# Kernel tuning notes

Hardware: AMD Instinct MI355X
Metric: run time of the kernel (lower is better)

Reference implementation:

```python
import jax, jax.numpy as jnp
import numpy as np

B, N, T = 512, 128, 64
ALPHA = 0.5  # LeakyReLU negative slope
NEG = jnp.float32(-9e15)


def _gat(h, mask, W, a):
    # GraphAttentionLayer with concat=True (trailing relu), eval mode (no dropout)
    Wh = h @ W                                   # [B,N,F]
    F = W.shape[1]
    e1 = Wh @ a[:F]                              # [B,N,1]
    e2 = Wh @ a[F:]                              # [B,N,1]
    e = jax.nn.leaky_relu(e1 + jnp.swapaxes(e2, 1, 2), ALPHA)  # [B,N,N]
    e = jnp.where(mask, e, NEG)
    att = jax.nn.softmax(e, axis=1)              # torch softmax dim=1 (over rows)
    return jax.nn.relu(jnp.matmul(att, Wh))


def _lstm_layer(x, wih, whh, bih, bhh):
    # x: [T,B,in]; hidden size 1; torch gate order i,f,g,o
    h0 = jnp.zeros((x.shape[1], 1), x.dtype)
    def step(carry, xt):
        h, c = carry
        g = xt @ wih.T + h @ whh.T + bih + bhh   # [B,4]
        i, f, gg, o = jnp.split(g, 4, axis=-1)
        c = jax.nn.sigmoid(f) * c + jax.nn.sigmoid(i) * jnp.tanh(gg)
        h = jax.nn.sigmoid(o) * jnp.tanh(c)
        return (h, c), h
    _, ys = jax.lax.scan(step, (h0, h0), x)
    return ys                                    # [T,B,1]


def setup_inputs() -> dict:
    key = jax.random.key(0)
    ks = jax.random.split(key, 32)
    def xu(k, shape, gain=1.414):
        lim = gain * np.sqrt(6.0 / (shape[0] + shape[1]))
        return jax.random.uniform(k, shape, jnp.float32, -lim, lim)
    d = {}
    d["adjacency"] = jax.random.randint(ks[0], (B, N, N), 0, 2, dtype=jnp.int32)
    d["feature"] = jax.random.normal(ks[1], (B, N), jnp.float32)
    d["time"] = jax.random.normal(ks[2], (B, N), jnp.float32)
    d["interval_popularity"] = jax.random.normal(ks[3], (B, T), jnp.float32)
    # GAT params
    d["W1"] = xu(ks[4], (1, 512)); d["a1"] = xu(ks[5], (1024, 1))
    d["W2"] = xu(ks[6], (512, 8)); d["a2"] = xu(ks[7], (16, 1))
    # attention-pooling params (torch.randn in original)
    d["Weight"] = jax.random.normal(ks[8], (128, 128), jnp.float32)
    d["Wv"] = jax.random.normal(ks[9], (128, 128), jnp.float32)
    # 2-layer LSTM(1->1)
    d["wih0"] = jax.random.normal(ks[10], (4, 1)) * 0.5
    d["whh0"] = jax.random.normal(ks[11], (4, 1)) * 0.5
    d["bih0"] = jax.random.normal(ks[12], (4,)) * 0.5
    d["bhh0"] = jax.random.normal(ks[13], (4,)) * 0.5
    d["wih1"] = jax.random.normal(ks[14], (4, 1)) * 0.5
    d["whh1"] = jax.random.normal(ks[15], (4, 1)) * 0.5
    d["bih1"] = jax.random.normal(ks[16], (4,)) * 0.5
    d["bhh1"] = jax.random.normal(ks[17], (4,)) * 0.5
    # MultiheadAttention(embed_dim=1, heads=1)
    d["mha_in_w"] = jax.random.normal(ks[18], (3, 1)) * 0.5
    d["mha_in_b"] = jnp.zeros((3,), jnp.float32)
    d["mha_out_w"] = jax.random.normal(ks[19], (1, 1)) * 0.5
    d["mha_out_b"] = jnp.zeros((1,), jnp.float32)
    # FL MLP: 192->128->32->1 (stored as [in,out])
    d["fl1_w"] = xu(ks[20], (192, 128), 1.0); d["fl1_b"] = jnp.zeros((128,), jnp.float32)
    d["fl2_w"] = xu(ks[21], (128, 32), 1.0);  d["fl2_b"] = jnp.zeros((32,), jnp.float32)
    d["fl3_w"] = xu(ks[22], (32, 1), 1.0);    d["fl3_b"] = jnp.zeros((1,), jnp.float32)
    return d


def reference(adjacency, feature, time, interval_popularity,
              W1, a1, W2, a2, Weight, Wv,
              wih0, whh0, bih0, bhh0, wih1, whh1, bih1, bhh1,
              mha_in_w, mha_in_b, mha_out_w, mha_out_b,
              fl1_w, fl1_b, fl2_w, fl2_b, fl3_w, fl3_b):
    mask = adjacency > 0
    x = feature.reshape(B, N, -1)                # [B,128,1]
    h = _gat(x, mask, W1, a1)                    # [B,128,512]
    h = jax.nn.relu(h)
    h = _gat(h, mask, W2, a2)                    # [B,128,8]

    xs = jnp.swapaxes(interval_popularity.reshape(B, -1, 1), 0, 1)  # [T,B,1]
    xs = _lstm_layer(xs, wih0, whh0, bih0, bhh0)
    xs = _lstm_layer(xs, wih1, whh1, bih1, bhh1)
    ip = jnp.swapaxes(xs, 0, 1).reshape(B, -1)   # [B,64]

    h = jnp.mean(h, axis=2, keepdims=True)       # [B,128,1]
    Wt = time.reshape(B, N, -1)                  # [B,128,1]
    att = jnp.concatenate([h, Wt], axis=2)       # [B,128,2]
    att = jnp.swapaxes(jnp.swapaxes(att, 1, 2) @ Weight, 1, 2)  # [B,128,2]
    att = jax.nn.softmax(att, axis=2)
    hv = jnp.swapaxes(jnp.concatenate([h, Wt], axis=2), 1, 2)   # [B,2,128]
    hv = jax.nn.relu((hv @ Wv).reshape(B, N, -1))  # faithful reshape (not transpose)
    h = jnp.sum(hv * att, axis=2)                # [B,128]

    h = jnp.concatenate([h, ip], axis=1)         # [B,192]
    hq = h[..., None]                            # [B,192,1]
    q = hq * mha_in_w[0, 0] + mha_in_b[0]
    k = hq * mha_in_w[1, 0] + mha_in_b[1]
    v = hq * mha_in_w[2, 0] + mha_in_b[2]
    a = jax.nn.softmax(q @ jnp.swapaxes(k, 1, 2), axis=-1)  # scale=1/sqrt(1)
    ho = (a @ v) * mha_out_w[0, 0] + mha_out_b[0]
    h = (ho + hq).reshape(B, -1)                 # [B,192]

    h = jax.nn.relu(h @ fl1_w + fl1_b)
    h = jnp.tanh(h @ fl2_w + fl2_b)
    h = jax.nn.relu(h @ fl3_w + fl3_b)           # [B,1]
    return h
```

## Files before the change

kernel.cpp:

```cpp
#include <hip/hip_runtime.h>
#include <math.h>

typedef unsigned int uint;
typedef unsigned long long ull;

#define L2E 1.44269504f

__device__ __forceinline__ float lrelu(float z){ return fmaxf(z, 0.5f*z); }
__device__ __forceinline__ float reluf(float z){ return fmaxf(z, 0.f); }
__device__ __forceinline__ float fexp(float z){ return __builtin_amdgcn_exp2f(z*L2E); }
__device__ __forceinline__ float frcp(float z){ return __builtin_amdgcn_rcpf(z); }
__device__ __forceinline__ float tanh_n(float z){
  return __fmaf_rn(2.f, __builtin_amdgcn_rcpf(1.f + __builtin_amdgcn_exp2f(-2.f*L2E*z)), -1.f);
}

__global__ __launch_bounds__(256) void pack_prep_kernel(
    const int* __restrict__ adj, ull* __restrict__ gpk, ull* __restrict__ gpkT,
    const float* __restrict__ W1, const float* __restrict__ a1,
    const float* __restrict__ W2, const float* __restrict__ a2,
    float* __restrict__ consts,
    const float* __restrict__ ipop,
    const float* __restrict__ wih0, const float* __restrict__ whh0,
    const float* __restrict__ bih0, const float* __restrict__ bhh0,
    const float* __restrict__ wih1, const float* __restrict__ whh1,
    const float* __restrict__ bih1, const float* __restrict__ bhh1,
    float* __restrict__ ip_out)
{
  const int bid = blockIdx.x, t = threadIdx.x;

  if (bid < 512){
    __shared__ ull rowW[256];
    const int w = t >> 6, ln = t & 63;
    const int* abase = adj + (((long)bid) << 14) + w*4096 + ln;
    ull myword = 0;
    #pragma unroll
    for (int blk = 0; blk < 8; ++blk){
      int v[8];
      #pragma unroll
      for (int q = 0; q < 8; ++q) v[q] = abase[(blk*8 + q)*64];
      #pragma unroll
      for (int q = 0; q < 8; ++q){
        ull m = __ballot(v[q] > 0);
        const int it = blk*8 + q;
        myword = (ln == it) ? m : myword;
      }
    }
    rowW[t] = myword;
    gpk[bid*256 + t] = myword;
    __syncthreads();
    const int j = t & 127, h2 = t >> 7;
    const int wsel = j >> 6, bsel = j & 63;
    ull outw = 0;
    #pragma unroll 8
    for (int k = 0; k < 64; ++k){
      outw |= ((rowW[(64*h2 + k)*2 + wsel] >> bsel) & 1ull) << k;
    }
    gpkT[bid*256 + j*2 + h2] = outw;
    return;
  }
  if (bid < 520){
    if (t >= 64) return;
    const int b = (bid - 512)*64 + t;
    float wi0[4], wh0[4], bb0[4], wi1[4], wh1[4], bb1[4];
    #pragma unroll
    for (int k = 0; k < 4; ++k){
      const float s = (k == 2) ? -2.f*L2E : -L2E;
      wi0[k]=wih0[k]*s; wh0[k]=whh0[k]*s; bb0[k]=(bih0[k]+bhh0[k])*s;
      wi1[k]=wih1[k]*s; wh1[k]=whh1[k]*s; bb1[k]=(bih1[k]+bhh1[k])*s;
    }
    const float4* xsrc = (const float4*)(ipop + b*64);
    float4* hdst = (float4*)(ip_out + b*64);
    float4 xv = xsrc[0];
    float h1=0.f, c1v=0.f, h2=0.f, c2v=0.f;
    #pragma unroll
    for (int q = 0; q < 16; ++q){
      const float4 xc = xv;
      if (q < 15) xv = xsrc[q+1];
      float hout[4];
      #pragma unroll
      for (int s = 0; s < 4; ++s){
        const float x = (s==0) ? xc.x : (s==1) ? xc.y : (s==2) ? xc.z : xc.w;
        float gi = frcp(1.f + __builtin_amdgcn_exp2f(__fmaf_rn(x, wi0[0], __fmaf_rn(h1, wh0[0], bb0[0]))));
        float gf = frcp(1.f + __builtin_amdgcn_exp2f(__fmaf_rn(x, wi0[1], __fmaf_rn(h1, wh0[1], bb0[1]))));
        float gg = __fmaf_rn(2.f, frcp(1.f + __builtin_amdgcn_exp2f(__fmaf_rn(x, wi0[2], __fmaf_rn(h1, wh0[2], bb0[2])))), -1.f);
        float go = frcp(1.f + __builtin_amdgcn_exp2f(__fmaf_rn(x, wi0[3], __fmaf_rn(h1, wh0[3], bb0[3]))));
        c1v = gf*c1v + gi*gg;
        h1 = go*tanh_n(c1v);
        float hi2 = frcp(1.f + __builtin_amdgcn_exp2f(__fmaf_rn(h1, wi1[0], __fmaf_rn(h2, wh1[0], bb1[0]))));
        float hf2 = frcp(1.f + __builtin_amdgcn_exp2f(__fmaf_rn(h1, wi1[1], __fmaf_rn(h2, wh1[1], bb1[1]))));
        float hg2 = __fmaf_rn(2.f, frcp(1.f + __builtin_amdgcn_exp2f(__fmaf_rn(h1, wi1[2], __fmaf_rn(h2, wh1[2], bb1[2])))), -1.f);
        float ho2 = frcp(1.f + __builtin_amdgcn_exp2f(__fmaf_rn(h1, wi1[3], __fmaf_rn(h2, wh1[3], bb1[3]))));
        c2v = hf2*c2v + hi2*hg2;
        h2 = ho2*tanh_n(c2v);
        hout[s] = h2;
      }
      hdst[q] = make_float4(hout[0], hout[1], hout[2], hout[3]);
    }
    return;
  }
  {
    __shared__ float redA[256], redB[256];
    float s1 = 0.f, s2 = 0.f;
    for (int f = t; f < 512; f += 256){ float w = W1[f]; s1 += w*a1[f]; s2 += w*a1[512+f]; }
    redA[t] = s1; redB[t] = s2; __syncthreads();
    for (int st = 128; st > 0; st >>= 1){
      if (t < st){ redA[t] += redA[t+st]; redB[t] += redB[t+st]; }
      __syncthreads();
    }
    if (t == 0){ consts[0] = redA[0]; consts[1] = redB[0]; }
    __syncthreads();
    const int g = t >> 5, seg = t & 31;
    float accP = 0.f, accQ = 0.f;
    for (int k = 0; k < 16; ++k){
      int f = seg*16 + k;
      float w = W1[f];
      float v = w * W2[f*8 + g];
      if (w > 0.f) accP += v; else accQ += v;
    }
    redA[t] = accP; redB[t] = accQ; __syncthreads();
    for (int st = 16; st > 0; st >>= 1){
      if (seg < st){ redA[t] += redA[t+st]; redB[t] += redB[t+st]; }
      __syncthreads();
    }
    if (seg == 0){ consts[2+g] = redA[t]; consts[10+g] = redB[t]; }
    __syncthreads();
    if (t == 0){
      float pA=0.f,qA=0.f,pB=0.f,qB=0.f;
      for (int gg = 0; gg < 8; ++gg){
        pA += consts[2+gg]*a2[gg];   qA += consts[10+gg]*a2[gg];
        pB += consts[2+gg]*a2[8+gg]; qB += consts[10+gg]*a2[8+gg];
      }
      consts[18]=pA; consts[19]=qA; consts[20]=pB; consts[21]=qB;
    }
  }
}

__global__ __launch_bounds__(256) void gat_head_kernel(
    const ull* __restrict__ gpk, const ull* __restrict__ gpkT,
    const float* __restrict__ feat, const float* __restrict__ timei,
    const float* __restrict__ Weight, const float* __restrict__ Wv,
    const float* __restrict__ consts, const float* __restrict__ ip,
    const float* __restrict__ mha_in_w, const float* __restrict__ mha_in_b,
    const float* __restrict__ mha_out_w, const float* __restrict__ mha_out_b,
    const float* __restrict__ fl1_w, const float* __restrict__ fl1_b,
    const float* __restrict__ fl2_w, const float* __restrict__ fl2_b,
    const float* __restrict__ fl3_w, const float* __restrict__ fl3_b,
    float* __restrict__ out)
{
  const int b = blockIdx.x, t = threadIdx.x;
  const int lane = t & 127, h = t >> 7;

  __shared__ float  xs[128], tim[128], hm[128], eAs[128], thr1[128];
  __shared__ float2 f2a[128];
  __shared__ float2 red2[2][128];
  __shared__ float4 q4[128];
  __shared__ float4 pool4[2][128];
  __shared__ float2 kv[192];
  __shared__ float  hq[192], h2s[192];
  __shared__ float  sred[8];

  const float c1 = consts[0], c2 = consts[1];
  const float pA = consts[18], qA = consts[19], pB = consts[20], qB = consts[21];

  float ipreg = 0.f;
  if (t < 128){ xs[t] = feat[b*128 + t]; tim[t] = timei[b*128 + t]; }
  if (t >= 192) ipreg = ip[b*64 + (t - 192)];
  const ull rowm = gpk [b*256 + lane*2 + h];
  const ull colm = gpkT[b*256 + lane*2 + h];
  __syncthreads();
  if (t < 64){
    float mx = fmaxf(xs[t], xs[t+64]);
    float mn = fminf(xs[t], xs[t+64]);
    #pragma unroll
    for (int off = 32; off; off >>= 1){
      mx = fmaxf(mx, __shfl_xor(mx, off));
      mn = fminf(mn, __shfl_xor(mn, off));
    }
    if (t == 0){ sred[0] = mx; sred[1] = mn; }
  }
  __syncthreads();

  float myE1=0.f, myEh=0.f, myA=0.f, myB=0.f, mythr=0.f, myx=0.f;
  {
    const float rmax = (c1 >= 0.f) ? c1*sred[0] : c1*sred[1];
    if (t < 128){
      myx = xs[t];
      float r  = c1*myx;
      float cj = c2*myx;
      float cb = lrelu(rmax + cj);
      myE1  = fexp(r - rmax);
      myEh  = fexp(0.5f*(r - rmax));
      myA   = fexp(rmax + cj - cb);
      myB   = fexp(0.5f*(rmax + cj) - cb);
      mythr = fexp(-cj - rmax);
      f2a[t] = make_float2(myE1, myEh);
      thr1[t] = mythr;
    }
  }
  __syncthreads();

  {
    const float thrj = thr1[lane];
    float s1 = 0.f, s2 = 0.f;
    #pragma unroll 8
    for (int k = 0; k < 64; ++k){
      float2 E = f2a[64*h + k];
      bool m = ((colm >> k) & 1ull);
      bool cond = (E.x >= thrj);
      s1 += (m &&  cond) ? E.x : 0.f;
      s2 += (m && !cond) ? E.y : 0.f;
    }
    red2[h][lane] = make_float2(s1, s2);
  }
  __syncthreads();
  if (t < 128){
    float2 a = red2[0][t], bb = red2[1][t];
    float den = __fmaf_rn(myA, a.x + bb.x, myB*(a.y + bb.y));
    float cr = frcp(den);
    q4[t] = make_float4(myA*cr*myx, myB*cr*myx, mythr, 0.f);
  }
  __syncthreads();
  {
    const float2 Eo = f2a[lane];
    float t1 = 0.f, t2 = 0.f;
    #pragma unroll 8
    for (int k = 0; k < 64; ++k){
      float4 G = q4[64*h + k];
      bool m = ((rowm >> k) & 1ull);
      bool cond = (Eo.x >= G.z);
      t1 += (m &&  cond) ? G.x : 0.f;
      t2 += (m && !cond) ? G.y : 0.f;
    }
    red2[h][lane] = make_float2(t1, t2);
  }
  __syncthreads();
  float u = 0.f, eBv = 0.f, eAv = 0.f;
  if (t < 128){
    float2 a = red2[0][t], bb = red2[1][t];
    u = __fmaf_rn(myE1, a.x + bb.x, myEh*(a.y + bb.y));
    eAv = (u >= 0.f ? pA : qA)*u;
    eBv = (u >= 0.f ? pB : qB)*u;
    eAs[t] = eAv;
  }
  __syncthreads();
  if (t < 64){
    float mx = fmaxf(eAs[t], eAs[t+64]);
    #pragma unroll
    for (int off = 32; off; off >>= 1) mx = fmaxf(mx, __shfl_xor(mx, off));
    if (t == 0) sred[2] = mx;
  }
  __syncthreads();
  float myE1b=0.f, myEhb=0.f, myA2=0.f, myB2=0.f;
  {
    const float eAmax = sred[2];
    if (t < 128){
      float cb = lrelu(eAmax + eBv);
      myE1b = fexp(eAv - eAmax);
      myEhb = fexp(0.5f*(eAv - eAmax));
      myA2  = fexp(eAmax + eBv - cb);
      myB2  = fexp(0.5f*(eAmax + eBv) - cb);
      float th = fexp(-eBv - eAmax);
      f2a[t] = make_float2(myE1b, myEhb);
      thr1[t] = th;
    }
  }
  __syncthreads();
  {
    const float thrj = thr1[lane];
    float s1 = 0.f, s2 = 0.f;
    #pragma unroll 8
    for (int k = 0; k < 64; ++k){
      float2 E = f2a[64*h + k];
      bool m = ((colm >> k) & 1ull);
      bool cond = (E.x >= thrj);
      s1 += (m &&  cond) ? E.x : 0.f;
      s2 += (m && !cond) ? E.y : 0.f;
    }
    red2[h][lane] = make_float2(s1, s2);
  }
  __syncthreads();
  if (t < 128){
    float2 a = red2[0][t], bb = red2[1][t];
    float den = __fmaf_rn(myA2, a.x + bb.x, myB2*(a.y + bb.y));
    float cr = frcp(den);
    float up = fmaxf(u, 0.f), un = fminf(u, 0.f);
    q4[t] = make_float4(myA2*cr*up, myB2*cr*up, myA2*cr*un, myB2*cr*un);
  }
  __syncthreads();
  {
    const float2 Eo = f2a[lane];
    float sp1=0.f, sp2=0.f, sn1=0.f, sn2=0.f;
    #pragma unroll 8
    for (int k = 0; k < 64; ++k){
      int j = 64*h + k;
      float4 G = q4[j];
      float thj = thr1[j];
      bool m = ((rowm >> k) & 1ull);
      bool cond = (Eo.x >= thj);
      sp1 += (m &&  cond) ? G.x : 0.f;
      sp2 += (m && !cond) ? G.y : 0.f;
      sn1 += (m &&  cond) ? G.z : 0.f;
      sn2 += (m && !cond) ? G.w : 0.f;
    }
    pool4[h][lane] = make_float4(sp1, sp2, sn1, sn2);
  }
  __syncthreads();
  if (t < 128){
    float4 a = pool4[0][t], bb = pool4[1][t];
    float sp = __fmaf_rn(myE1b, a.x + bb.x, myEhb*(a.y + bb.y));
    float sn = __fmaf_rn(myE1b, a.z + bb.z, myEhb*(a.w + bb.w));
    float acc = 0.f;
    #pragma unroll
    for (int g = 0; g < 8; ++g) acc += reluf(__fmaf_rn(sp, consts[2+g], sn*consts[10+g]));
    hm[t] = 0.125f*acc;
  }
  __syncthreads();

  {
    const int n = lane;
    float a0=0.f, a1v=0.f, v0=0.f, v1=0.f;
    const int m0 = h*64;
    #pragma unroll 4
    for (int k = 0; k < 64; ++k){
      int m = m0 + k;
      float hmv = hm[m], tv = tim[m];
      float wg = Weight[(m<<7) + n], wvv = Wv[(m<<7) + n];
      a0 = __fmaf_rn(hmv, wg, a0); a1v = __fmaf_rn(tv, wg, a1v);
      v0 = __fmaf_rn(hmv, wvv, v0); v1 = __fmaf_rn(tv, wvv, v1);
    }
    pool4[h][n] = make_float4(a0, a1v, v0, v1);
  }
  __syncthreads();
  float att0 = 0.f, att1 = 0.f, rsv = 0.f;
  if (t < 128){
    float4 a = pool4[0][t], bb = pool4[1][t];
    float A0 = a.x + bb.x, A1 = a.y + bb.y;
    red2[0][t] = make_float2(a.z + bb.z, a.w + bb.w);
    float mx = fmaxf(A0, A1);
    att0 = fexp(A0 - mx); att1 = fexp(A1 - mx);
    rsv = frcp(att0 + att1);
  }
  __syncthreads();
  if (t < 128){
    float r0, r1;
    if (t < 64){ r0 = red2[0][2*t].x;     r1 = red2[0][2*t+1].x; }
    else       { r0 = red2[0][2*t-128].y; r1 = red2[0][2*t-127].y; }
    hq[t] = (reluf(r0)*att0 + reluf(r1)*att1)*rsv;
  }
  if (t >= 192) hq[128 + (t - 192)] = ipreg;
  __syncthreads();

  const float wq = mha_in_w[0], wk = mha_in_w[1], wv = mha_in_w[2];
  const float bq = mha_in_b[0], bk = mha_in_b[1], bv = mha_in_b[2];
  const float wo = mha_out_w[0], bo = mha_out_b[0];
  if (t < 192){
    float hv_ = hq[t];
    kv[t] = make_float2(__fmaf_rn(hv_, wk, bk), __fmaf_rn(hv_, wv, bv));
  }
  __syncthreads();
  if (t < 64){
    float k0 = kv[t].x, k1 = kv[t+64].x, k2 = kv[t+128].x;
    float mx = fmaxf(fmaxf(k0, k1), k2);
    float mn = fminf(fminf(k0, k1), k2);
    #pragma unroll
    for (int off = 32; off; off >>= 1){
      mx = fmaxf(mx, __shfl_xor(mx, off));
      mn = fminf(mn, __shfl_xor(mn, off));
    }
    if (t == 0){ sred[3] = mx; sred[4] = mn; }
  }
  __syncthreads();
  if (t < 192){
    float hv_ = hq[t];
    float qi = __fmaf_rn(hv_, wq, bq);
    float mx = (qi >= 0.f) ? qi*sred[3] : qi*sred[4];
    const float qi2 = qi*L2E, mx2 = mx*L2E;
    float den = 0.f, num = 0.f;
    #pragma unroll 8
    for (int j = 0; j < 192; ++j){
      float2 K = kv[j];
      float e = __builtin_amdgcn_exp2f(__fmaf_rn(qi2, K.x, -mx2));
      den += e; num = __fmaf_rn(e, K.y, num);
    }
    h2s[t] = __fmaf_rn(num*frcp(den), wo, bo) + hv_;
  }
  __syncthreads();
  {
    const int n = t & 127;
    float acc = 0.f;
    const int i0 = h*96;
    #pragma unroll 8
    for (int k = 0; k < 96; ++k){
      int i = i0 + k;
      acc = __fmaf_rn(h2s[i], fl1_w[i*128 + n], acc);
    }
    red2[h][n].x = acc;
  }
  __syncthreads();
  if (t < 128) thr1[t] = reluf(red2[0][t].x + red2[1][t].x + fl1_b[t]);
  __syncthreads();
  if (t < 128){
    const int n = t & 31, seg = t >> 5;
    float p = 0.f;
    #pragma unroll 8
    for (int k = 0; k < 32; ++k){
      int i = seg*32 + k;
      p = __fmaf_rn(thr1[i], fl2_w[i*32 + n], p);
    }
    eAs[t] = p;
  }
  __syncthreads();
  if (t < 32) hm[t] = tanh_n(eAs[t] + eAs[t+32] + eAs[t+64] + eAs[t+96] + fl2_b[t]);
  __syncthreads();
  if (t < 64){
    float p = (t < 32) ? hm[t]*fl3_w[t] : 0.f;
    #pragma unroll
    for (int off = 32; off; off >>= 1) p += __shfl_xor(p, off);
    if (t == 0) out[b] = reluf(p + fl3_b[0]);
  }
}

extern "C" void kernel_launch(void* const* d_in, const int* in_sizes, int n_in,
                              void* d_out, int out_size, void* d_ws, size_t ws_size,
                              hipStream_t stream) {
  const int*   adj    = (const int*)  d_in[0];
  const float* feat   = (const float*)d_in[1];
  const float* timei  = (const float*)d_in[2];
  const float* ipop   = (const float*)d_in[3];
  const float* W1     = (const float*)d_in[4];
  const float* a1     = (const float*)d_in[5];
  const float* W2     = (const float*)d_in[6];
  const float* a2     = (const float*)d_in[7];
  const float* Weight = (const float*)d_in[8];
  const float* Wv     = (const float*)d_in[9];
  const float* wih0   = (const float*)d_in[10];
  const float* whh0   = (const float*)d_in[11];
  const float* bih0   = (const float*)d_in[12];
  const float* bhh0   = (const float*)d_in[13];
  const float* wih1   = (const float*)d_in[14];
  const float* whh1   = (const float*)d_in[15];
  const float* bih1   = (const float*)d_in[16];
  const float* bhh1   = (const float*)d_in[17];
  const float* mha_in_w  = (const float*)d_in[18];
  const float* mha_in_b  = (const float*)d_in[19];
  const float* mha_out_w = (const float*)d_in[20];
  const float* mha_out_b = (const float*)d_in[21];
  const float* fl1_w = (const float*)d_in[22];
  const float* fl1_b = (const float*)d_in[23];
  const float* fl2_w = (const float*)d_in[24];
  const float* fl2_b = (const float*)d_in[25];
  const float* fl3_w = (const float*)d_in[26];
  const float* fl3_b = (const float*)d_in[27];

  ull*   gpk    = (ull*)d_ws;
  ull*   gpkT   = gpk + 131072;
  float* consts = (float*)(gpkT + 131072);
  float* ip     = consts + 32;

  pack_prep_kernel<<<521, 256, 0, stream>>>(adj, gpk, gpkT, W1, a1, W2, a2, consts,
                                            ipop, wih0, whh0, bih0, bhh0,
                                            wih1, whh1, bih1, bhh1, ip);
  gat_head_kernel<<<512, 256, 0, stream>>>(gpk, gpkT, feat, timei, Weight, Wv, consts, ip,
                                           mha_in_w, mha_in_b, mha_out_w, mha_out_b,
                                           fl1_w, fl1_b, fl2_w, fl2_b, fl3_w, fl3_b,
                                           (float*)d_out);
}
```

Baseline: 49.82 us.

## Fuse pack, prep, LSTM and GAT head into one kernel

Merges the adjacency bit-packing, the GAT constant precompute, the LSTM recurrence and the GAT/head computation into a single kernel, one block per batch. The packed masks stay in shared memory instead of being written to and re-read from the workspace, which also removes a kernel launch and the dependency between the two kernels. Each block recomputes the tiny weight-derived constants with wave shuffles, and one thread runs the LSTM in eight 8-step chunks placed between the GAT barriers so it overlaps the GAT work. The trade-offs are redundant constant computation in every block, and a serial LSTM on a single lane that could stretch the barrier phases it is interleaved with.

```diff
diff --git a/kernel.cpp b/kernel.cpp
--- a/kernel.cpp
+++ b/kernel.cpp
@@ -14,132 +14,17 @@
   return __fmaf_rn(2.f, __builtin_amdgcn_rcpf(1.f + __builtin_amdgcn_exp2f(-2.f*L2E*z)), -1.f);
 }
 
-__global__ __launch_bounds__(256) void pack_prep_kernel(
-    const int* __restrict__ adj, ull* __restrict__ gpk, ull* __restrict__ gpkT,
+__global__ __launch_bounds__(256) void fused_kernel(
+    const int* __restrict__ adj, const float* __restrict__ feat,
+    const float* __restrict__ timei,
+    const float* __restrict__ Weight, const float* __restrict__ Wv,
     const float* __restrict__ W1, const float* __restrict__ a1,
     const float* __restrict__ W2, const float* __restrict__ a2,
-    float* __restrict__ consts,
     const float* __restrict__ ipop,
     const float* __restrict__ wih0, const float* __restrict__ whh0,
     const float* __restrict__ bih0, const float* __restrict__ bhh0,
     const float* __restrict__ wih1, const float* __restrict__ whh1,
     const float* __restrict__ bih1, const float* __restrict__ bhh1,
-    float* __restrict__ ip_out)
-{
-  const int bid = blockIdx.x, t = threadIdx.x;
-
-  if (bid < 512){
-    __shared__ ull rowW[256];
-    const int w = t >> 6, ln = t & 63;
-    const int* abase = adj + (((long)bid) << 14) + w*4096 + ln;
-    ull myword = 0;
-    #pragma unroll
-    for (int blk = 0; blk < 8; ++blk){
-      int v[8];
-      #pragma unroll
-      for (int q = 0; q < 8; ++q) v[q] = abase[(blk*8 + q)*64];
-      #pragma unroll
-      for (int q = 0; q < 8; ++q){
-        ull m = __ballot(v[q] > 0);
-        const int it = blk*8 + q;
-        myword = (ln == it) ? m : myword;
-      }
-    }
-    rowW[t] = myword;
-    gpk[bid*256 + t] = myword;
-    __syncthreads();
-    const int j = t & 127, h2 = t >> 7;
-    const int wsel = j >> 6, bsel = j & 63;
-    ull outw = 0;
-    #pragma unroll 8
-    for (int k = 0; k < 64; ++k){
-      outw |= ((rowW[(64*h2 + k)*2 + wsel] >> bsel) & 1ull) << k;
-    }
-    gpkT[bid*256 + j*2 + h2] = outw;
-    return;
-  }
-  if (bid < 520){
-    if (t >= 64) return;
-    const int b = (bid - 512)*64 + t;
-    float wi0[4], wh0[4], bb0[4], wi1[4], wh1[4], bb1[4];
-    #pragma unroll
-    for (int k = 0; k < 4; ++k){
-      const float s = (k == 2) ? -2.f*L2E : -L2E;
-      wi0[k]=wih0[k]*s; wh0[k]=whh0[k]*s; bb0[k]=(bih0[k]+bhh0[k])*s;
-      wi1[k]=wih1[k]*s; wh1[k]=whh1[k]*s; bb1[k]=(bih1[k]+bhh1[k])*s;
-    }
-    const float4* xsrc = (const float4*)(ipop + b*64);
-    float4* hdst = (float4*)(ip_out + b*64);
-    float4 xv = xsrc[0];
-    float h1=0.f, c1v=0.f, h2=0.f, c2v=0.f;
-    #pragma unroll
-    for (int q = 0; q < 16; ++q){
-      const float4 xc = xv;
-      if (q < 15) xv = xsrc[q+1];
-      float hout[4];
-      #pragma unroll
-      for (int s = 0; s < 4; ++s){
-        const float x = (s==0) ? xc.x : (s==1) ? xc.y : (s==2) ? xc.z : xc.w;
-        float gi = frcp(1.f + __builtin_amdgcn_exp2f(__fmaf_rn(x, wi0[0], __fmaf_rn(h1, wh0[0], bb0[0]))));
-        float gf = frcp(1.f + __builtin_amdgcn_exp2f(__fmaf_rn(x, wi0[1], __fmaf_rn(h1, wh0[1], bb0[1]))));
-        float gg = __fmaf_rn(2.f, frcp(1.f + __builtin_amdgcn_exp2f(__fmaf_rn(x, wi0[2], __fmaf_rn(h1, wh0[2], bb0[2])))), -1.f);
-        float go = frcp(1.f + __builtin_amdgcn_exp2f(__fmaf_rn(x, wi0[3], __fmaf_rn(h1, wh0[3], bb0[3]))));
-        c1v = gf*c1v + gi*gg;
-        h1 = go*tanh_n(c1v);
-        float hi2 = frcp(1.f + __builtin_amdgcn_exp2f(__fmaf_rn(h1, wi1[0], __fmaf_rn(h2, wh1[0], bb1[0]))));
-        float hf2 = frcp(1.f + __builtin_amdgcn_exp2f(__fmaf_rn(h1, wi1[1], __fmaf_rn(h2, wh1[1], bb1[1]))));
-        float hg2 = __fmaf_rn(2.f, frcp(1.f + __builtin_amdgcn_exp2f(__fmaf_rn(h1, wi1[2], __fmaf_rn(h2, wh1[2], bb1[2])))), -1.f);
-        float ho2 = frcp(1.f + __builtin_amdgcn_exp2f(__fmaf_rn(h1, wi1[3], __fmaf_rn(h2, wh1[3], bb1[3]))));
-        c2v = hf2*c2v + hi2*hg2;
-        h2 = ho2*tanh_n(c2v);
-        hout[s] = h2;
-      }
-      hdst[q] = make_float4(hout[0], hout[1], hout[2], hout[3]);
-    }
-    return;
-  }
-  {
-    __shared__ float redA[256], redB[256];
-    float s1 = 0.f, s2 = 0.f;
-    for (int f = t; f < 512; f += 256){ float w = W1[f]; s1 += w*a1[f]; s2 += w*a1[512+f]; }
-    redA[t] = s1; redB[t] = s2; __syncthreads();
-    for (int st = 128; st > 0; st >>= 1){
-      if (t < st){ redA[t] += redA[t+st]; redB[t] += redB[t+st]; }
-      __syncthreads();
-    }
-    if (t == 0){ consts[0] = redA[0]; consts[1] = redB[0]; }
-    __syncthreads();
-    const int g = t >> 5, seg = t & 31;
-    float accP = 0.f, accQ = 0.f;
-    for (int k = 0; k < 16; ++k){
-      int f = seg*16 + k;
-      float w = W1[f];
-      float v = w * W2[f*8 + g];
-      if (w > 0.f) accP += v; else accQ += v;
-    }
-    redA[t] = accP; redB[t] = accQ; __syncthreads();
-    for (int st = 16; st > 0; st >>= 1){
-      if (seg < st){ redA[t] += redA[t+st]; redB[t] += redB[t+st]; }
-      __syncthreads();
-    }
-    if (seg == 0){ consts[2+g] = redA[t]; consts[10+g] = redB[t]; }
-    __syncthreads();
-    if (t == 0){
-      float pA=0.f,qA=0.f,pB=0.f,qB=0.f;
-      for (int gg = 0; gg < 8; ++gg){
-        pA += consts[2+gg]*a2[gg];   qA += consts[10+gg]*a2[gg];
-        pB += consts[2+gg]*a2[8+gg]; qB += consts[10+gg]*a2[8+gg];
-      }
-      consts[18]=pA; consts[19]=qA; consts[20]=pB; consts[21]=qB;
-    }
-  }
-}
-
-__global__ __launch_bounds__(256) void gat_head_kernel(
-    const ull* __restrict__ gpk, const ull* __restrict__ gpkT,
-    const float* __restrict__ feat, const float* __restrict__ timei,
-    const float* __restrict__ Weight, const float* __restrict__ Wv,
-    const float* __restrict__ consts, const float* __restrict__ ip,
     const float* __restrict__ mha_in_w, const float* __restrict__ mha_in_b,
     const float* __restrict__ mha_out_w, const float* __restrict__ mha_out_b,
     const float* __restrict__ fl1_w, const float* __restrict__ fl1_b,
@@ -149,8 +34,10 @@
 {
   const int b = blockIdx.x, t = threadIdx.x;
   const int lane = t & 127, h = t >> 7;
-
-  __shared__ float  xs[128], tim[128], hm[128], eAs[128], thr1[128];
+  const int wv = t >> 6, ln = t & 63;
+
+  __shared__ ull   rowW[256];
+  __shared__ float xs[128], tim[128], hm[128], eAs[128], thr1[128];
   __shared__ float2 f2a[128];
   __shared__ float2 red2[2][128];
   __shared__ float4 q4[128];
@@ -158,16 +45,120 @@
   __shared__ float2 kv[192];
   __shared__ float  hq[192], h2s[192];
   __shared__ float  sred[8];
-
-  const float c1 = consts[0], c2 = consts[1];
-  const float pA = consts[18], qA = consts[19], pB = consts[20], qB = consts[21];
-
-  float ipreg = 0.f;
+  __shared__ float  cpart[4][2];
+  __shared__ float  pqpart[4][16];
+  __shared__ float  cons[24];
+  __shared__ float  ips[64];
+
   if (t < 128){ xs[t] = feat[b*128 + t]; tim[t] = timei[b*128 + t]; }
-  if (t >= 192) ipreg = ip[b*64 + (t - 192)];
-  const ull rowm = gpk [b*256 + lane*2 + h];
-  const ull colm = gpkT[b*256 + lane*2 + h];
-  __syncthreads();
+
+  float a2reg[16];
+  if (t == 0){
+    #pragma unroll
+    for (int g = 0; g < 16; ++g) a2reg[g] = a2[g];
+  }
+
+  float h1v=0.f, c1s=0.f, h2v=0.f, c2s=0.f;
+  float wi0s[4], wh0s[4], bb0s[4], wi1s[4], wh1s[4], bb1s[4];
+  const float4* xsrc4 = (const float4*)(ipop + b*64);
+  float4 xcur0, xcur1;
+  if (t == 255){
+    #pragma unroll
+    for (int k = 0; k < 4; ++k){
+      const float s = (k == 2) ? -2.f*L2E : -L2E;
+      wi0s[k]=wih0[k]*s; wh0s[k]=whh0[k]*s; bb0s[k]=(bih0[k]+bhh0[k])*s;
+      wi1s[k]=wih1[k]*s; wh1s[k]=whh1[k]*s; bb1s[k]=(bih1[k]+bhh1[k])*s;
+    }
+    xcur0 = xsrc4[0]; xcur1 = xsrc4[1];
+  }
+  auto lstm8 = [&](int c){
+    if (t != 255) return;
+    const float4 xa = xcur0, xb = xcur1;
+    if (c < 7){ xcur0 = xsrc4[2*c+2]; xcur1 = xsrc4[2*c+3]; }
+    float o[8];
+    #pragma unroll
+    for (int si = 0; si < 8; ++si){
+      const float x = (si==0)?xa.x:(si==1)?xa.y:(si==2)?xa.z:(si==3)?xa.w:
+                      (si==4)?xb.x:(si==5)?xb.y:(si==6)?xb.z:xb.w;
+      float gi = frcp(1.f + __builtin_amdgcn_exp2f(__fmaf_rn(x, wi0s[0], __fmaf_rn(h1v, wh0s[0], bb0s[0]))));
+      float gf = frcp(1.f + __builtin_amdgcn_exp2f(__fmaf_rn(x, wi0s[1], __fmaf_rn(h1v, wh0s[1], bb0s[1]))));
+      float gg = __fmaf_rn(2.f, frcp(1.f + __builtin_amdgcn_exp2f(__fmaf_rn(x, wi0s[2], __fmaf_rn(h1v, wh0s[2], bb0s[2])))), -1.f);
+      float go = frcp(1.f + __builtin_amdgcn_exp2f(__fmaf_rn(x, wi0s[3], __fmaf_rn(h1v, wh0s[3], bb0s[3]))));
+      c1s = gf*c1s + gi*gg;  h1v = go*tanh_n(c1s);
+      float hi = frcp(1.f + __builtin_amdgcn_exp2f(__fmaf_rn(h1v, wi1s[0], __fmaf_rn(h2v, wh1s[0], bb1s[0]))));
+      float hf = frcp(1.f + __builtin_amdgcn_exp2f(__fmaf_rn(h1v, wi1s[1], __fmaf_rn(h2v, wh1s[1], bb1s[1]))));
+      float hg = __fmaf_rn(2.f, frcp(1.f + __builtin_amdgcn_exp2f(__fmaf_rn(h1v, wi1s[2], __fmaf_rn(h2v, wh1s[2], bb1s[2])))), -1.f);
+      float ho = frcp(1.f + __builtin_amdgcn_exp2f(__fmaf_rn(h1v, wi1s[3], __fmaf_rn(h2v, wh1s[3], bb1s[3]))));
+      c2s = hf*c2s + hi*hg;  h2v = ho*tanh_n(c2s);
+      o[si] = h2v;
+    }
+    #pragma unroll
+    for (int si = 0; si < 8; ++si) ips[8*c + si] = o[si];
+  };
+
+  {
+    const int* abase = adj + (((long)b) << 14) + wv*4096 + ln;
+    ull myword = 0;
+    #pragma unroll
+    for (int blk = 0; blk < 8; ++blk){
+      int v[8];
+      #pragma unroll
+      for (int q = 0; q < 8; ++q) v[q] = abase[(blk*8 + q)*64];
+      #pragma unroll
+      for (int q = 0; q < 8; ++q){
+        ull m = __ballot(v[q] > 0);
+        myword = (ln == blk*8 + q) ? m : myword;
+      }
+    }
+    rowW[t] = myword;
+  }
+
+  {
+    float w0 = W1[t], w1 = W1[t+256];
+    float s1 = __fmaf_rn(w0, a1[t],     w1*a1[t+256]);
+    float s2 = __fmaf_rn(w0, a1[512+t], w1*a1[768+t]);
+    #pragma unroll
+    for (int off = 32; off; off >>= 1){ s1 += __shfl_xor(s1, off); s2 += __shfl_xor(s2, off); }
+    if (ln == 0){ cpart[wv][0] = s1; cpart[wv][1] = s2; }
+  }
+  {
+    float accP[8], accQ[8];
+    #pragma unroll
+    for (int g = 0; g < 8; ++g){ accP[g] = 0.f; accQ[g] = 0.f; }
+    #pragma unroll
+    for (int e = 0; e < 2; ++e){
+      const int f = 2*t + e;
+      const float w = W1[f];
+      const float wp = fmaxf(w, 0.f), wn = fminf(w, 0.f);
+      const float4 A = *(const float4*)(W2 + f*8);
+      const float4 Bv = *(const float4*)(W2 + f*8 + 4);
+      accP[0]=__fmaf_rn(wp,A.x,accP[0]);  accQ[0]=__fmaf_rn(wn,A.x,accQ[0]);
+      accP[1]=__fmaf_rn(wp,A.y,accP[1]);  accQ[1]=__fmaf_rn(wn,A.y,accQ[1]);
+      accP[2]=__fmaf_rn(wp,A.z,accP[2]);  accQ[2]=__fmaf_rn(wn,A.z,accQ[2]);
+      accP[3]=__fmaf_rn(wp,A.w,accP[3]);  accQ[3]=__fmaf_rn(wn,A.w,accQ[3]);
+      accP[4]=__fmaf_rn(wp,Bv.x,accP[4]); accQ[4]=__fmaf_rn(wn,Bv.x,accQ[4]);
+      accP[5]=__fmaf_rn(wp,Bv.y,accP[5]); accQ[5]=__fmaf_rn(wn,Bv.y,accQ[5]);
+      accP[6]=__fmaf_rn(wp,Bv.z,accP[6]); accQ[6]=__fmaf_rn(wn,Bv.z,accQ[6]);
+      accP[7]=__fmaf_rn(wp,Bv.w,accP[7]); accQ[7]=__fmaf_rn(wn,Bv.w,accQ[7]);
+    }
+    #pragma unroll
+    for (int g = 0; g < 8; ++g){
+      float p = accP[g], q = accQ[g];
+      #pragma unroll
+      for (int off = 32; off; off >>= 1){ p += __shfl_xor(p, off); q += __shfl_xor(q, off); }
+      if (ln == 0){ pqpart[wv][g] = p; pqpart[wv][8+g] = q; }
+    }
+  }
+  __syncthreads();
+
+  const ull rowm = rowW[lane*2 + h];
+  ull colm = 0;
+  {
+    const int wsel = lane >> 6, bsel = lane & 63;
+    #pragma unroll 8
+    for (int k = 0; k < 64; ++k)
+      colm |= ((rowW[(64*h + k)*2 + wsel] >> bsel) & 1ull) << k;
+  }
   if (t < 64){
     float mx = fmaxf(xs[t], xs[t+64]);
     float mn = fminf(xs[t], xs[t+64]);
@@ -178,10 +169,27 @@
     }
     if (t == 0){ sred[0] = mx; sred[1] = mn; }
   }
+  if (t == 0){
+    float c1v = cpart[0][0]+cpart[1][0]+cpart[2][0]+cpart[3][0];
+    float c2v = cpart[0][1]+cpart[1][1]+cpart[2][1]+cpart[3][1];
+    cons[0] = c1v; cons[1] = c2v;
+    float pAx=0.f, qAx=0.f, pBx=0.f, qBx=0.f;
+    #pragma unroll
+    for (int g = 0; g < 8; ++g){
+      float P = pqpart[0][g]+pqpart[1][g]+pqpart[2][g]+pqpart[3][g];
+      float Q = pqpart[0][8+g]+pqpart[1][8+g]+pqpart[2][8+g]+pqpart[3][8+g];
+      cons[2+g] = P; cons[10+g] = Q;
+      pAx = __fmaf_rn(P, a2reg[g],   pAx);  qAx = __fmaf_rn(Q, a2reg[g],   qAx);
+      pBx = __fmaf_rn(P, a2reg[8+g], pBx);  qBx = __fmaf_rn(Q, a2reg[8+g], qBx);
+    }
+    cons[18]=pAx; cons[19]=qAx; cons[20]=pBx; cons[21]=qBx;
+  }
+  lstm8(0);
   __syncthreads();
 
   float myE1=0.f, myEh=0.f, myA=0.f, myB=0.f, mythr=0.f, myx=0.f;
   {
+    const float c1 = cons[0], c2 = cons[1];
     const float rmax = (c1 >= 0.f) ? c1*sred[0] : c1*sred[1];
     if (t < 128){
       myx = xs[t];
@@ -197,6 +205,7 @@
       thr1[t] = mythr;
     }
   }
+  lstm8(1);
   __syncthreads();
 
   {
@@ -212,14 +221,18 @@
     }
     red2[h][lane] = make_float2(s1, s2);
   }
-  __syncthreads();
+  lstm8(2);
+  __syncthreads();
+
   if (t < 128){
     float2 a = red2[0][t], bb = red2[1][t];
     float den = __fmaf_rn(myA, a.x + bb.x, myB*(a.y + bb.y));
     float cr = frcp(den);
     q4[t] = make_float4(myA*cr*myx, myB*cr*myx, mythr, 0.f);
   }
-  __syncthreads();
+  lstm8(3);
+  __syncthreads();
+
   {
     const float2 Eo = f2a[lane];
     float t1 = 0.f, t2 = 0.f;
@@ -233,23 +246,29 @@
     }
     red2[h][lane] = make_float2(t1, t2);
   }
-  __syncthreads();
+  lstm8(4);
+  __syncthreads();
+
   float u = 0.f, eBv = 0.f, eAv = 0.f;
   if (t < 128){
     float2 a = red2[0][t], bb = red2[1][t];
     u = __fmaf_rn(myE1, a.x + bb.x, myEh*(a.y + bb.y));
-    eAv = (u >= 0.f ? pA : qA)*u;
-    eBv = (u >= 0.f ? pB : qB)*u;
+    eAv = (u >= 0.f ? cons[18] : cons[19])*u;
+    eBv = (u >= 0.f ? cons[20] : cons[21])*u;
     eAs[t] = eAv;
   }
-  __syncthreads();
+  lstm8(5);
+  __syncthreads();
+
   if (t < 64){
     float mx = fmaxf(eAs[t], eAs[t+64]);
     #pragma unroll
     for (int off = 32; off; off >>= 1) mx = fmaxf(mx, __shfl_xor(mx, off));
     if (t == 0) sred[2] = mx;
   }
-  __syncthreads();
+  lstm8(6);
+  __syncthreads();
+
   float myE1b=0.f, myEhb=0.f, myA2=0.f, myB2=0.f;
   {
     const float eAmax = sred[2];
@@ -264,7 +283,9 @@
       thr1[t] = th;
     }
   }
-  __syncthreads();
+  lstm8(7);
+  __syncthreads();
+
   {
     const float thrj = thr1[lane];
     float s1 = 0.f, s2 = 0.f;
@@ -279,6 +300,7 @@
     red2[h][lane] = make_float2(s1, s2);
   }
   __syncthreads();
+
   if (t < 128){
     float2 a = red2[0][t], bb = red2[1][t];
     float den = __fmaf_rn(myA2, a.x + bb.x, myB2*(a.y + bb.y));
@@ -287,6 +309,7 @@
     q4[t] = make_float4(myA2*cr*up, myB2*cr*up, myA2*cr*un, myB2*cr*un);
   }
   __syncthreads();
+
   {
     const float2 Eo = f2a[lane];
     float sp1=0.f, sp2=0.f, sn1=0.f, sn2=0.f;
@@ -305,13 +328,14 @@
     pool4[h][lane] = make_float4(sp1, sp2, sn1, sn2);
   }
   __syncthreads();
+
   if (t < 128){
     float4 a = pool4[0][t], bb = pool4[1][t];
     float sp = __fmaf_rn(myE1b, a.x + bb.x, myEhb*(a.y + bb.y));
     float sn = __fmaf_rn(myE1b, a.z + bb.z, myEhb*(a.w + bb.w));
     float acc = 0.f;
     #pragma unroll
-    for (int g = 0; g < 8; ++g) acc += reluf(__fmaf_rn(sp, consts[2+g], sn*consts[10+g]));
+    for (int g = 0; g < 8; ++g) acc += reluf(__fmaf_rn(sp, cons[2+g], sn*cons[10+g]));
     hm[t] = 0.125f*acc;
   }
   __syncthreads();
@@ -331,6 +355,7 @@
     pool4[h][n] = make_float4(a0, a1v, v0, v1);
   }
   __syncthreads();
+
   float att0 = 0.f, att1 = 0.f, rsv = 0.f;
   if (t < 128){
     float4 a = pool4[0][t], bb = pool4[1][t];
@@ -341,23 +366,25 @@
     rsv = frcp(att0 + att1);
   }
   __syncthreads();
+
   if (t < 128){
     float r0, r1;
     if (t < 64){ r0 = red2[0][2*t].x;     r1 = red2[0][2*t+1].x; }
     else       { r0 = red2[0][2*t-128].y; r1 = red2[0][2*t-127].y; }
     hq[t] = (reluf(r0)*att0 + reluf(r1)*att1)*rsv;
   }
-  if (t >= 192) hq[128 + (t - 192)] = ipreg;
-  __syncthreads();
-
-  const float wq = mha_in_w[0], wk = mha_in_w[1], wv = mha_in_w[2];
+  if (t >= 192) hq[128 + (t - 192)] = ips[t - 192];
+  __syncthreads();
+
+  const float wq = mha_in_w[0], wk = mha_in_w[1], wvv_ = mha_in_w[2];
   const float bq = mha_in_b[0], bk = mha_in_b[1], bv = mha_in_b[2];
   const float wo = mha_out_w[0], bo = mha_out_b[0];
   if (t < 192){
     float hv_ = hq[t];
-    kv[t] = make_float2(__fmaf_rn(hv_, wk, bk), __fmaf_rn(hv_, wv, bv));
-  }
-  __syncthreads();
+    kv[t] = make_float2(__fmaf_rn(hv_, wk, bk), __fmaf_rn(hv_, wvv_, bv));
+  }
+  __syncthreads();
+
   if (t < 64){
     float k0 = kv[t].x, k1 = kv[t+64].x, k2 = kv[t+128].x;
     float mx = fmaxf(fmaxf(k0, k1), k2);
@@ -370,6 +397,7 @@
     if (t == 0){ sred[3] = mx; sred[4] = mn; }
   }
   __syncthreads();
+
   if (t < 192){
     float hv_ = hq[t];
     float qi = __fmaf_rn(hv_, wq, bq);
@@ -385,6 +413,7 @@
     h2s[t] = __fmaf_rn(num*frcp(den), wo, bo) + hv_;
   }
   __syncthreads();
+
   {
     const int n = t & 127;
     float acc = 0.f;
@@ -397,8 +426,10 @@
     red2[h][n].x = acc;
   }
   __syncthreads();
+
   if (t < 128) thr1[t] = reluf(red2[0][t].x + red2[1][t].x + fl1_b[t]);
   __syncthreads();
+
   if (t < 128){
     const int n = t & 31, seg = t >> 5;
     float p = 0.f;
@@ -410,8 +441,10 @@
     eAs[t] = p;
   }
   __syncthreads();
+
   if (t < 32) hm[t] = tanh_n(eAs[t] + eAs[t+32] + eAs[t+64] + eAs[t+96] + fl2_b[t]);
   __syncthreads();
+
   if (t < 64){
     float p = (t < 32) ? hm[t]*fl3_w[t] : 0.f;
     #pragma unroll
@@ -452,16 +485,11 @@
   const float* fl3_w = (const float*)d_in[26];
   const float* fl3_b = (const float*)d_in[27];
 
-  ull*   gpk    = (ull*)d_ws;
-  ull*   gpkT   = gpk + 131072;
-  float* consts = (float*)(gpkT + 131072);
-  float* ip     = consts + 32;
-
-  pack_prep_kernel<<<521, 256, 0, stream>>>(adj, gpk, gpkT, W1, a1, W2, a2, consts,
-                                            ipop, wih0, whh0, bih0, bhh0,
-                                            wih1, whh1, bih1, bhh1, ip);
-  gat_head_kernel<<<512, 256, 0, stream>>>(gpk, gpkT, feat, timei, Weight, Wv, consts, ip,
-                                           mha_in_w, mha_in_b, mha_out_w, mha_out_b,
-                                           fl1_w, fl1_b, fl2_w, fl2_b, fl3_w, fl3_b,
-                                           (float*)d_out);
+  fused_kernel<<<512, 256, 0, stream>>>(adj, feat, timei, Weight, Wv,
+                                        W1, a1, W2, a2, ipop,
+                                        wih0, whh0, bih0, bhh0,
+                                        wih1, whh1, bih1, bhh1,
+                                        mha_in_w, mha_in_b, mha_out_w, mha_out_b,
+                                        fl1_w, fl1_b, fl2_w, fl2_b, fl3_w, fl3_b,
+                                        (float*)d_out);
 }
```

Result: no change. 49.36 us (-0.9%).
